# Kernel tuning notes

Hardware: AMD Instinct MI355X
Metric: run time of the kernel (lower is better)

The kernel has to match this reference:

```python
import jax, jax.numpy as jnp
import numpy as np

B, Q, D = 8, 1, 4096
NH, NKV, HD = 32, 8, 128
KV = 4096
ROPE_BASE = 10000.0


def setup_inputs() -> dict:
    key = jax.random.key(0)
    ks = jax.random.split(key, 10)
    s = 0.02  # realistic init scale for weights
    return {
        "hidden_states": jax.random.normal(ks[0], (B, Q, D), jnp.float32),
        "past_k": jax.random.normal(ks[1], (B, NH, KV, HD), jnp.float32),
        "past_v": jax.random.normal(ks[2], (B, NH, KV, HD), jnp.float32),
        "Wq": jax.random.normal(ks[3], (NH * HD, D), jnp.float32) * s,
        "bq": jax.random.normal(ks[4], (NH * HD,), jnp.float32) * s,
        "Wk": jax.random.normal(ks[5], (NKV * HD, D), jnp.float32) * s,
        "bk": jax.random.normal(ks[6], (NKV * HD,), jnp.float32) * s,
        "Wv": jax.random.normal(ks[7], (NKV * HD, D), jnp.float32) * s,
        "bv": jax.random.normal(ks[8], (NKV * HD,), jnp.float32) * s,
        "Wo": jax.random.normal(ks[9], (D, NH * HD), jnp.float32) * s,
        "position_ids": KV,  # current decode position (past length)
    }


def _rope(x, pos0):
    # x: [B, H, Q, HD]; rotate_half-style RoPE at positions pos0..pos0+Q-1
    half = HD // 2
    inv_freq = 1.0 / (ROPE_BASE ** (jnp.arange(half, dtype=jnp.float32) / half))
    pos = (pos0 + jnp.arange(Q)).astype(jnp.float32)          # [Q]
    ang = pos[:, None] * inv_freq[None, :]                    # [Q, half]
    cos = jnp.concatenate([jnp.cos(ang), jnp.cos(ang)], -1)   # [Q, HD]
    sin = jnp.concatenate([jnp.sin(ang), jnp.sin(ang)], -1)
    x1, x2 = x[..., :half], x[..., half:]
    rot = jnp.concatenate([-x2, x1], axis=-1)
    return x * cos + rot * sin


def reference(hidden_states, past_k, past_v, Wq, bq, Wk, bk, Wv, bv, Wo, position_ids):
    # QKV projections (Qwen: biased q/k/v, unbiased o)
    q = hidden_states @ Wq.T + bq   # [B, Q, NH*HD]
    k = hidden_states @ Wk.T + bk   # [B, Q, NKV*HD]
    v = hidden_states @ Wv.T + bv
    q = q.reshape(B, Q, NH, HD).transpose(0, 2, 1, 3)    # [B, NH, Q, HD]
    k = k.reshape(B, Q, NKV, HD).transpose(0, 2, 1, 3)   # [B, NKV, Q, HD]
    v = v.reshape(B, Q, NKV, HD).transpose(0, 2, 1, 3)
    # RoPE on current tokens only (past cache already rotated)
    q = _rope(q, position_ids)
    k = _rope(k, position_ids)
    # GQA repeat_interleave to full head count
    rep = NH // NKV
    k = jnp.repeat(k, rep, axis=1)   # [B, NH, Q, HD]
    v = jnp.repeat(v, rep, axis=1)
    # Assemble streaming KV window: past cache is stored post-repeat
    k = jnp.concatenate([past_k, k], axis=2)   # [B, NH, KV+Q, HD]
    v = jnp.concatenate([past_v, v], axis=2)
    scale = jnp.float32(1.0 / np.sqrt(HD))
    scores = jnp.einsum("bhqd,bhkd->bhqk", q, k) * scale   # [B, NH, Q, KV+Q]
    # causal: query positions KV..KV+Q-1 attend to key positions <= own pos
    qpos = KV + jnp.arange(Q)
    kpos = jnp.arange(KV + Q)
    mask = qpos[:, None] >= kpos[None, :]
    scores = jnp.where(mask, scores, jnp.float32(-1e30))
    attn = jax.nn.softmax(scores, axis=-1)
    ctx = jnp.einsum("bhqk,bhkd->bhqd", attn, v)           # [B, NH, Q, HD]
    ctx = ctx.transpose(0, 2, 1, 3).reshape(B, Q, NH * HD)
    return ctx @ Wo.T   # [B, Q, D]
```

## Files before the change

kernel.cpp:

```cpp
#include <hip/hip_runtime.h>
#include <hip/hip_bf16.h>
#include <math.h>

#define BB 8
#define DD 4096
#define NH 32
#define NKV 8
#define HD 128
#define KVL 4096
#define NSPLIT 16
#define CHUNK (KVL / NSPLIT)
#define SCALE 0.08838834764831845f

#define OFF_QRAW  0
#define OFF_KRAW  (OFF_QRAW + BB*NH*HD)
#define OFF_VRAW  (OFF_KRAW + BB*NKV*HD)
#define OFF_QROPE (OFF_VRAW + BB*NKV*HD)
#define OFF_KROPE (OFF_QROPE + BB*NH*HD)
#define OFF_PART  (OFF_KROPE + BB*NKV*HD)
#define PART_STRIDE 132
#define OFF_CTX   (OFF_PART + BB*NH*NSPLIT*PART_STRIDE)

__global__ __launch_bounds__(256) void k_qkv(
    const float* __restrict__ hs,
    const float* __restrict__ Wq, const float* __restrict__ bq,
    const float* __restrict__ Wk, const float* __restrict__ bk,
    const float* __restrict__ Wv, const float* __restrict__ bv,
    float* __restrict__ ws)
{
    const int wid  = threadIdx.x >> 6;
    const int lane = threadIdx.x & 63;
    const int row  = blockIdx.x * 4 + wid;
    const float* W; const float* bias; float* dst; int dstride; int r;
    if (row < 4096)      { W = Wq; bias = bq; r = row;        dst = ws + OFF_QRAW; dstride = NH*HD; }
    else if (row < 5120) { W = Wk; bias = bk; r = row - 4096; dst = ws + OFF_KRAW; dstride = NKV*HD; }
    else                 { W = Wv; bias = bv; r = row - 5120; dst = ws + OFF_VRAW; dstride = NKV*HD; }

    const float4* Wr = (const float4*)(W + (size_t)r * DD);
    float acc[BB];
    #pragma unroll
    for (int b = 0; b < BB; ++b) acc[b] = 0.f;

    for (int it = 0; it < DD/256; ++it) {
        const int idx = it*64 + lane;
        const float4 w4 = Wr[idx];
        #pragma unroll
        for (int b = 0; b < BB; ++b) {
            const float4 h4 = ((const float4*)(hs + (size_t)b*DD))[idx];
            acc[b] = fmaf(w4.x, h4.x, fmaf(w4.y, h4.y, fmaf(w4.z, h4.z, fmaf(w4.w, h4.w, acc[b]))));
        }
    }
    #pragma unroll
    for (int b = 0; b < BB; ++b) {
        float v = acc[b];
        #pragma unroll
        for (int off = 32; off; off >>= 1) v += __shfl_xor(v, off, 64);
        acc[b] = v;
    }
    if (lane == 0) {
        const float bb = bias[r];
        #pragma unroll
        for (int b = 0; b < BB; ++b) dst[(size_t)b*dstride + r] = acc[b] + bb;
    }
}

__global__ __launch_bounds__(256) void k_rope(const int* __restrict__ posp, float* __restrict__ ws)
{
    const int gid = blockIdx.x * 256 + threadIdx.x;
    const int i  = gid & (HD-1);
    const int hh = gid >> 7;
    const double pos = (double)posp[0];
    const int j = i & 63;
    const double ang = pos * pow(10000.0, -(double)j / 64.0);
    const float c = (float)cos(ang), s = (float)sin(ang);
    const bool isq = hh < BB*NH;
    const int hl = isq ? hh : hh - BB*NH;
    const float* src = ws + (isq ? OFF_QRAW  : OFF_KRAW)  + hl * HD;
    float* dstp      = ws + (isq ? OFF_QROPE : OFF_KROPE) + hl * HD;
    const float x = src[i];
    const float o = (i < 64) ? -src[i + 64] : src[i - 64];
    dstp[i] = fmaf(x, c, o * s);
}

__global__ __launch_bounds__(256) void k_attn(
    const float* __restrict__ Kc, const float* __restrict__ Vc,
    float* __restrict__ ws)
{
    __shared__ float sc[CHUNK + 1];
    __shared__ float red[4];
    __shared__ float ctxs[HD];

    const int pair  = blockIdx.x / NSPLIT;
    const int split = blockIdx.x % NSPLIT;
    const int b = pair >> 5, h = pair & 31;
    const int tid = threadIdx.x, wid = tid >> 6, lane = tid & 63;
    const int sub = lane >> 5, l32 = lane & 31;

    const float* q = ws + OFF_QROPE + pair * HD;
    const size_t base = ((size_t)pair * KVL + (size_t)split * CHUNK) * HD;
    const float* Kp = Kc + base;
    const float* Vp = Vc + base;
    const bool extra = (split == NSPLIT - 1);

    const float4 q4 = ((const float4*)q)[l32];

    #pragma unroll 4
    for (int it = 0; it < 32; ++it) {
        const int p = wid*64 + it*2 + sub;
        const float4 k4 = ((const float4*)(Kp + (size_t)p * HD))[l32];
        float v = q4.x*k4.x + q4.y*k4.y + q4.z*k4.z + q4.w*k4.w;
        #pragma unroll
        for (int off = 16; off; off >>= 1) v += __shfl_xor(v, off, 64);
        if (l32 == 0) sc[p] = v * SCALE;
    }
    if (extra && wid == 0) {
        const float* kn = ws + OFF_KROPE + (b*NKV + (h>>2)) * HD;
        const float4 k4 = ((const float4*)kn)[l32];
        float v = q4.x*k4.x + q4.y*k4.y + q4.z*k4.z + q4.w*k4.w;
        #pragma unroll
        for (int off = 16; off; off >>= 1) v += __shfl_xor(v, off, 64);
        if (lane == 0) sc[CHUNK] = v * SCALE;
    }
    __syncthreads();

    const int cnt = CHUNK + (extra ? 1 : 0);
    float m = -1e30f;
    for (int p2 = tid; p2 < cnt; p2 += 256) m = fmaxf(m, sc[p2]);
    #pragma unroll
    for (int off = 32; off; off >>= 1) m = fmaxf(m, __shfl_xor(m, off, 64));
    if (lane == 0) red[wid] = m;
    __syncthreads();
    m = fmaxf(fmaxf(red[0], red[1]), fmaxf(red[2], red[3]));
    __syncthreads();
    float lsum = 0.f;
    for (int p2 = tid; p2 < cnt; p2 += 256) {
        const float e = expf(sc[p2] - m);
        sc[p2] = e;
        lsum += e;
    }
    #pragma unroll
    for (int off = 32; off; off >>= 1) lsum += __shfl_xor(lsum, off, 64);
    if (lane == 0) red[wid] = lsum;
    __syncthreads();
    const float L = red[0] + red[1] + red[2] + red[3];

    const int d = tid & (HD-1);
    const int half = tid >> 7;
    float acc = 0.f;
    const float* Vh = Vp + (size_t)half * (CHUNK/2) * HD;
    for (int i2 = 0; i2 < CHUNK/2; ++i2)
        acc = fmaf(sc[half*(CHUNK/2) + i2], Vh[(size_t)i2 * HD + d], acc);
    if (extra && half == 0) {
        const float* vn = ws + OFF_VRAW + (b*NKV + (h>>2)) * HD;
        acc = fmaf(sc[CHUNK], vn[d], acc);
    }
    if (half == 0) ctxs[d] = acc;
    __syncthreads();
    if (half == 1) ctxs[d] += acc;
    __syncthreads();

    float* pp = ws + OFF_PART + ((size_t)pair * NSPLIT + split) * PART_STRIDE;
    if (tid < HD)            pp[tid]    = ctxs[tid];
    else if (tid == HD)      pp[HD]     = m;
    else if (tid == HD + 1)  pp[HD + 1] = L;
}

__global__ __launch_bounds__(128) void k_combine(float* __restrict__ ws)
{
    const int pair = blockIdx.x;
    const int d = threadIdx.x;
    const float* pp = ws + OFF_PART + (size_t)pair * NSPLIT * PART_STRIDE;
    __shared__ float sm[NSPLIT], sl[NSPLIT];
    if (d < NSPLIT) { sm[d] = pp[d*PART_STRIDE + HD]; sl[d] = pp[d*PART_STRIDE + HD + 1]; }
    __syncthreads();
    float M = -1e30f;
    #pragma unroll
    for (int s = 0; s < NSPLIT; ++s) M = fmaxf(M, sm[s]);
    float L = 0.f, acc = 0.f;
    #pragma unroll
    for (int s = 0; s < NSPLIT; ++s) {
        const float w = expf(sm[s] - M);
        L += sl[s] * w;
        acc += pp[s*PART_STRIDE + d] * w;
    }
    ws[OFF_CTX + pair*HD + d] = acc / L;
}

__global__ __launch_bounds__(256) void k_oproj(
    const float* __restrict__ Wo, const float* __restrict__ ws, float* __restrict__ out)
{
    const int wid  = threadIdx.x >> 6;
    const int lane = threadIdx.x & 63;
    const int row  = blockIdx.x * 4 + wid;
    const float4* Wr = (const float4*)(Wo + (size_t)row * DD);
    const float* ctx = ws + OFF_CTX;
    float acc[BB];
    #pragma unroll
    for (int b = 0; b < BB; ++b) acc[b] = 0.f;
    for (int it = 0; it < DD/256; ++it) {
        const int idx = it*64 + lane;
        const float4 w4 = Wr[idx];
        #pragma unroll
        for (int b = 0; b < BB; ++b) {
            const float4 h4 = ((const float4*)(ctx + (size_t)b*DD))[idx];
            acc[b] = fmaf(w4.x, h4.x, fmaf(w4.y, h4.y, fmaf(w4.z, h4.z, fmaf(w4.w, h4.w, acc[b]))));
        }
    }
    #pragma unroll
    for (int b = 0; b < BB; ++b) {
        float v = acc[b];
        #pragma unroll
        for (int off = 32; off; off >>= 1) v += __shfl_xor(v, off, 64);
        if (lane == 0) out[(size_t)b*DD + row] = v;
    }
}

extern "C" void kernel_launch(void* const* d_in, const int* in_sizes, int n_in,
                              void* d_out, int out_size, void* d_ws, size_t ws_size,
                              hipStream_t stream)
{
    const float* hs  = (const float*)d_in[0];
    const float* pk  = (const float*)d_in[1];
    const float* pv  = (const float*)d_in[2];
    const float* Wq  = (const float*)d_in[3];
    const float* bq  = (const float*)d_in[4];
    const float* Wk  = (const float*)d_in[5];
    const float* bk  = (const float*)d_in[6];
    const float* Wv  = (const float*)d_in[7];
    const float* bv  = (const float*)d_in[8];
    const float* Wo  = (const float*)d_in[9];
    const int*   pos = (const int*)d_in[10];
    float* out = (float*)d_out;
    float* ws  = (float*)d_ws;

    k_qkv   <<<6144/4,           256, 0, stream>>>(hs, Wq, bq, Wk, bk, Wv, bv, ws);
    k_rope  <<<(BB*(NH+NKV)*HD)/256, 256, 0, stream>>>(pos, ws);
    k_attn  <<<BB*NH*NSPLIT,     256, 0, stream>>>(pk, pv, ws);
    k_combine<<<BB*NH,           128, 0, stream>>>(ws);
    k_oproj <<<4096/4,           256, 0, stream>>>(Wo, ws, out);
}
```

Before: 271.0 us.

## Fuse RoPE into QKV projection and use per-wave online-softmax attention

The QKV projection kernel now has each wave compute the paired rows i and i+64 of a head and apply RoPE in registers, so the separate RoPE kernel and its workspace round trip go away. Attention is rewritten so each wavefront handles one split of 128 keys with a single-pass online softmax, reading K and V together. This removes the shared-memory score buffer and the block-level barriers. NSPLIT doubles to 32, which adds more partials for the combine kernel to merge, and the online softmax adds rescaling branches inside the inner loop.

```diff
diff --git a/kernel.cpp b/kernel.cpp
--- a/kernel.cpp
+++ b/kernel.cpp
@@ -4,165 +4,170 @@
 
 #define BB 8
 #define DD 4096
-#define NH 32
+#define NHQ 32
 #define NKV 8
 #define HD 128
 #define KVL 4096
-#define NSPLIT 16
+#define NSPLIT 32
 #define CHUNK (KVL / NSPLIT)
 #define SCALE 0.08838834764831845f
 
-#define OFF_QRAW  0
-#define OFF_KRAW  (OFF_QRAW + BB*NH*HD)
-#define OFF_VRAW  (OFF_KRAW + BB*NKV*HD)
-#define OFF_QROPE (OFF_VRAW + BB*NKV*HD)
-#define OFF_KROPE (OFF_QROPE + BB*NH*HD)
-#define OFF_PART  (OFF_KROPE + BB*NKV*HD)
+#define OFF_QROPE 0
+#define OFF_KROPE (OFF_QROPE + BB*NHQ*HD)
+#define OFF_VRAW  (OFF_KROPE + BB*NKV*HD)
+#define OFF_PART  (OFF_VRAW  + BB*NKV*HD)
 #define PART_STRIDE 132
-#define OFF_CTX   (OFF_PART + BB*NH*NSPLIT*PART_STRIDE)
+#define OFF_CTX   (OFF_PART + BB*NHQ*NSPLIT*PART_STRIDE)
 
 __global__ __launch_bounds__(256) void k_qkv(
     const float* __restrict__ hs,
     const float* __restrict__ Wq, const float* __restrict__ bq,
     const float* __restrict__ Wk, const float* __restrict__ bk,
     const float* __restrict__ Wv, const float* __restrict__ bv,
+    const int* __restrict__ posp,
     float* __restrict__ ws)
 {
     const int wid  = threadIdx.x >> 6;
     const int lane = threadIdx.x & 63;
-    const int row  = blockIdx.x * 4 + wid;
-    const float* W; const float* bias; float* dst; int dstride; int r;
-    if (row < 4096)      { W = Wq; bias = bq; r = row;        dst = ws + OFF_QRAW; dstride = NH*HD; }
-    else if (row < 5120) { W = Wk; bias = bk; r = row - 4096; dst = ws + OFF_KRAW; dstride = NKV*HD; }
-    else                 { W = Wv; bias = bv; r = row - 5120; dst = ws + OFF_VRAW; dstride = NKV*HD; }
-
-    const float4* Wr = (const float4*)(W + (size_t)r * DD);
-    float acc[BB];
-    #pragma unroll
-    for (int b = 0; b < BB; ++b) acc[b] = 0.f;
+    const int w    = blockIdx.x * 4 + wid;
+
+    const float* W; const float* bias; float* dst; int dstride; int r1; int i; bool rope;
+    if (w < 2048) {
+        const int h = w >> 6; i = w & 63; r1 = h*HD + i;
+        W = Wq; bias = bq; dst = ws + OFF_QROPE; dstride = NHQ*HD; rope = true;
+    } else if (w < 2560) {
+        const int w2 = w - 2048; const int h = w2 >> 6; i = w2 & 63; r1 = h*HD + i;
+        W = Wk; bias = bk; dst = ws + OFF_KROPE; dstride = NKV*HD; rope = true;
+    } else {
+        const int w3 = w - 2560; const int h = w3 >> 6; i = w3 & 63; r1 = h*HD + i;
+        W = Wv; bias = bv; dst = ws + OFF_VRAW; dstride = NKV*HD; rope = false;
+    }
+    const int r2 = r1 + 64;
+
+    const double pos = (double)posp[0];
+    const double ang = pos * pow(10000.0, -(double)i / 64.0);
+    const float c = (float)cos(ang), s = (float)sin(ang);
+
+    const float4* WrA = (const float4*)(W + (size_t)r1 * DD);
+    const float4* WrB = (const float4*)(W + (size_t)r2 * DD);
+    const float4* H   = (const float4*)hs;
+
+    float accA[BB], accB[BB];
+    #pragma unroll
+    for (int b = 0; b < BB; ++b) { accA[b] = 0.f; accB[b] = 0.f; }
 
     for (int it = 0; it < DD/256; ++it) {
         const int idx = it*64 + lane;
-        const float4 w4 = Wr[idx];
+        const float4 wa = WrA[idx];
+        const float4 wb = WrB[idx];
         #pragma unroll
         for (int b = 0; b < BB; ++b) {
-            const float4 h4 = ((const float4*)(hs + (size_t)b*DD))[idx];
-            acc[b] = fmaf(w4.x, h4.x, fmaf(w4.y, h4.y, fmaf(w4.z, h4.z, fmaf(w4.w, h4.w, acc[b]))));
+            const float4 h4 = H[b*(DD/4) + idx];
+            accA[b] = fmaf(wa.x, h4.x, fmaf(wa.y, h4.y, fmaf(wa.z, h4.z, fmaf(wa.w, h4.w, accA[b]))));
+            accB[b] = fmaf(wb.x, h4.x, fmaf(wb.y, h4.y, fmaf(wb.z, h4.z, fmaf(wb.w, h4.w, accB[b]))));
         }
     }
     #pragma unroll
     for (int b = 0; b < BB; ++b) {
-        float v = acc[b];
-        #pragma unroll
-        for (int off = 32; off; off >>= 1) v += __shfl_xor(v, off, 64);
-        acc[b] = v;
+        float va = accA[b], vb = accB[b];
+        #pragma unroll
+        for (int off = 32; off; off >>= 1) {
+            va += __shfl_xor(va, off, 64);
+            vb += __shfl_xor(vb, off, 64);
+        }
+        accA[b] = va; accB[b] = vb;
     }
     if (lane == 0) {
-        const float bb = bias[r];
-        #pragma unroll
-        for (int b = 0; b < BB; ++b) dst[(size_t)b*dstride + r] = acc[b] + bb;
-    }
-}
-
-__global__ __launch_bounds__(256) void k_rope(const int* __restrict__ posp, float* __restrict__ ws)
-{
-    const int gid = blockIdx.x * 256 + threadIdx.x;
-    const int i  = gid & (HD-1);
-    const int hh = gid >> 7;
-    const double pos = (double)posp[0];
-    const int j = i & 63;
-    const double ang = pos * pow(10000.0, -(double)j / 64.0);
-    const float c = (float)cos(ang), s = (float)sin(ang);
-    const bool isq = hh < BB*NH;
-    const int hl = isq ? hh : hh - BB*NH;
-    const float* src = ws + (isq ? OFF_QRAW  : OFF_KRAW)  + hl * HD;
-    float* dstp      = ws + (isq ? OFF_QROPE : OFF_KROPE) + hl * HD;
-    const float x = src[i];
-    const float o = (i < 64) ? -src[i + 64] : src[i - 64];
-    dstp[i] = fmaf(x, c, o * s);
+        const float b1 = bias[r1], b2 = bias[r2];
+        #pragma unroll
+        for (int b = 0; b < BB; ++b) {
+            const float a1 = accA[b] + b1;
+            const float a2 = accB[b] + b2;
+            float o1, o2;
+            if (rope) { o1 = fmaf(a1, c, -a2*s); o2 = fmaf(a2, c, a1*s); }
+            else      { o1 = a1;                 o2 = a2; }
+            dst[(size_t)b*dstride + r1] = o1;
+            dst[(size_t)b*dstride + r2] = o2;
+        }
+    }
 }
 
 __global__ __launch_bounds__(256) void k_attn(
     const float* __restrict__ Kc, const float* __restrict__ Vc,
     float* __restrict__ ws)
 {
-    __shared__ float sc[CHUNK + 1];
-    __shared__ float red[4];
-    __shared__ float ctxs[HD];
-
-    const int pair  = blockIdx.x / NSPLIT;
-    const int split = blockIdx.x % NSPLIT;
+    const int wid  = threadIdx.x >> 6;
+    const int lane = threadIdx.x & 63;
+    const int sub  = lane >> 5, l32 = lane & 31;
+    const int task  = blockIdx.x * 4 + wid;
+    const int pair  = task >> 5;
+    const int split = task & (NSPLIT - 1);
     const int b = pair >> 5, h = pair & 31;
-    const int tid = threadIdx.x, wid = tid >> 6, lane = tid & 63;
-    const int sub = lane >> 5, l32 = lane & 31;
-
-    const float* q = ws + OFF_QROPE + pair * HD;
+
+    const float4 q4 = ((const float4*)(ws + OFF_QROPE + (size_t)pair * HD))[l32];
     const size_t base = ((size_t)pair * KVL + (size_t)split * CHUNK) * HD;
-    const float* Kp = Kc + base;
-    const float* Vp = Vc + base;
-    const bool extra = (split == NSPLIT - 1);
-
-    const float4 q4 = ((const float4*)q)[l32];
+    const float4* Kp = (const float4*)(Kc + base);
+    const float4* Vp = (const float4*)(Vc + base);
+
+    float m = -1e30f, l = 0.f;
+    float4 acc = {0.f, 0.f, 0.f, 0.f};
 
     #pragma unroll 4
-    for (int it = 0; it < 32; ++it) {
-        const int p = wid*64 + it*2 + sub;
-        const float4 k4 = ((const float4*)(Kp + (size_t)p * HD))[l32];
-        float v = q4.x*k4.x + q4.y*k4.y + q4.z*k4.z + q4.w*k4.w;
-        #pragma unroll
-        for (int off = 16; off; off >>= 1) v += __shfl_xor(v, off, 64);
-        if (l32 == 0) sc[p] = v * SCALE;
-    }
-    if (extra && wid == 0) {
-        const float* kn = ws + OFF_KROPE + (b*NKV + (h>>2)) * HD;
-        const float4 k4 = ((const float4*)kn)[l32];
-        float v = q4.x*k4.x + q4.y*k4.y + q4.z*k4.z + q4.w*k4.w;
-        #pragma unroll
-        for (int off = 16; off; off >>= 1) v += __shfl_xor(v, off, 64);
-        if (lane == 0) sc[CHUNK] = v * SCALE;
-    }
-    __syncthreads();
-
-    const int cnt = CHUNK + (extra ? 1 : 0);
-    float m = -1e30f;
-    for (int p2 = tid; p2 < cnt; p2 += 256) m = fmaxf(m, sc[p2]);
-    #pragma unroll
-    for (int off = 32; off; off >>= 1) m = fmaxf(m, __shfl_xor(m, off, 64));
-    if (lane == 0) red[wid] = m;
-    __syncthreads();
-    m = fmaxf(fmaxf(red[0], red[1]), fmaxf(red[2], red[3]));
-    __syncthreads();
-    float lsum = 0.f;
-    for (int p2 = tid; p2 < cnt; p2 += 256) {
-        const float e = expf(sc[p2] - m);
-        sc[p2] = e;
-        lsum += e;
-    }
-    #pragma unroll
-    for (int off = 32; off; off >>= 1) lsum += __shfl_xor(lsum, off, 64);
-    if (lane == 0) red[wid] = lsum;
-    __syncthreads();
-    const float L = red[0] + red[1] + red[2] + red[3];
-
-    const int d = tid & (HD-1);
-    const int half = tid >> 7;
-    float acc = 0.f;
-    const float* Vh = Vp + (size_t)half * (CHUNK/2) * HD;
-    for (int i2 = 0; i2 < CHUNK/2; ++i2)
-        acc = fmaf(sc[half*(CHUNK/2) + i2], Vh[(size_t)i2 * HD + d], acc);
-    if (extra && half == 0) {
-        const float* vn = ws + OFF_VRAW + (b*NKV + (h>>2)) * HD;
-        acc = fmaf(sc[CHUNK], vn[d], acc);
-    }
-    if (half == 0) ctxs[d] = acc;
-    __syncthreads();
-    if (half == 1) ctxs[d] += acc;
-    __syncthreads();
-
-    float* pp = ws + OFF_PART + ((size_t)pair * NSPLIT + split) * PART_STRIDE;
-    if (tid < HD)            pp[tid]    = ctxs[tid];
-    else if (tid == HD)      pp[HD]     = m;
-    else if (tid == HD + 1)  pp[HD + 1] = L;
+    for (int it = 0; it < CHUNK/2; ++it) {
+        const int p = it*2 + sub;
+        const float4 k4 = Kp[p*32 + l32];
+        const float4 v4 = Vp[p*32 + l32];
+        float sv = fmaf(q4.x, k4.x, fmaf(q4.y, k4.y, fmaf(q4.z, k4.z, q4.w*k4.w)));
+        #pragma unroll
+        for (int off = 16; off; off >>= 1) sv += __shfl_xor(sv, off, 64);
+        sv *= SCALE;
+        if (sv > m) {
+            const float r_ = __expf(m - sv);
+            l *= r_; acc.x *= r_; acc.y *= r_; acc.z *= r_; acc.w *= r_;
+            m = sv;
+        }
+        const float pw = __expf(sv - m);
+        l += pw;
+        acc.x = fmaf(pw, v4.x, acc.x);
+        acc.y = fmaf(pw, v4.y, acc.y);
+        acc.z = fmaf(pw, v4.z, acc.z);
+        acc.w = fmaf(pw, v4.w, acc.w);
+    }
+
+    if (split == NSPLIT - 1 && sub == 0) {
+        const float4 k4 = ((const float4*)(ws + OFF_KROPE + (size_t)(b*NKV + (h>>2)) * HD))[l32];
+        const float4 v4 = ((const float4*)(ws + OFF_VRAW  + (size_t)(b*NKV + (h>>2)) * HD))[l32];
+        float sv = fmaf(q4.x, k4.x, fmaf(q4.y, k4.y, fmaf(q4.z, k4.z, q4.w*k4.w)));
+        #pragma unroll
+        for (int off = 16; off; off >>= 1) sv += __shfl_xor(sv, off, 64);
+        sv *= SCALE;
+        if (sv > m) {
+            const float r_ = __expf(m - sv);
+            l *= r_; acc.x *= r_; acc.y *= r_; acc.z *= r_; acc.w *= r_;
+            m = sv;
+        }
+        const float pw = __expf(sv - m);
+        l += pw;
+        acc.x = fmaf(pw, v4.x, acc.x);
+        acc.y = fmaf(pw, v4.y, acc.y);
+        acc.z = fmaf(pw, v4.z, acc.z);
+        acc.w = fmaf(pw, v4.w, acc.w);
+    }
+
+    const float M  = fmaxf(m, __shfl_xor(m, 32, 64));
+    const float r_ = __expf(m - M);
+    l *= r_; acc.x *= r_; acc.y *= r_; acc.z *= r_; acc.w *= r_;
+    l     += __shfl_xor(l,     32, 64);
+    acc.x += __shfl_xor(acc.x, 32, 64);
+    acc.y += __shfl_xor(acc.y, 32, 64);
+    acc.z += __shfl_xor(acc.z, 32, 64);
+    acc.w += __shfl_xor(acc.w, 32, 64);
+
+    if (sub == 0) {
+        float* pp = ws + OFF_PART + ((size_t)pair * NSPLIT + split) * PART_STRIDE;
+        ((float4*)pp)[l32] = acc;
+        if (l32 == 0) { pp[HD] = M; pp[HD+1] = l; }
+    }
 }
 
 __global__ __launch_bounds__(128) void k_combine(float* __restrict__ ws)
@@ -181,9 +186,9 @@
     for (int s = 0; s < NSPLIT; ++s) {
         const float w = expf(sm[s] - M);
         L += sl[s] * w;
-        acc += pp[s*PART_STRIDE + d] * w;
-    }
-    ws[OFF_CTX + pair*HD + d] = acc / L;
+        acc = fmaf(pp[s*PART_STRIDE + d], w, acc);
+    }
+    ws[OFF_CTX + (size_t)pair*HD + d] = acc / L;
 }
 
 __global__ __launch_bounds__(256) void k_oproj(
@@ -193,7 +198,7 @@
     const int lane = threadIdx.x & 63;
     const int row  = blockIdx.x * 4 + wid;
     const float4* Wr = (const float4*)(Wo + (size_t)row * DD);
-    const float* ctx = ws + OFF_CTX;
+    const float4* C  = (const float4*)(ws + OFF_CTX);
     float acc[BB];
     #pragma unroll
     for (int b = 0; b < BB; ++b) acc[b] = 0.f;
@@ -202,7 +207,7 @@
         const float4 w4 = Wr[idx];
         #pragma unroll
         for (int b = 0; b < BB; ++b) {
-            const float4 h4 = ((const float4*)(ctx + (size_t)b*DD))[idx];
+            const float4 h4 = C[b*(DD/4) + idx];
             acc[b] = fmaf(w4.x, h4.x, fmaf(w4.y, h4.y, fmaf(w4.z, h4.z, fmaf(w4.w, h4.w, acc[b]))));
         }
     }
@@ -233,9 +238,8 @@
     float* out = (float*)d_out;
     float* ws  = (float*)d_ws;
 
-    k_qkv   <<<6144/4,           256, 0, stream>>>(hs, Wq, bq, Wk, bk, Wv, bv, ws);
-    k_rope  <<<(BB*(NH+NKV)*HD)/256, 256, 0, stream>>>(pos, ws);
-    k_attn  <<<BB*NH*NSPLIT,     256, 0, stream>>>(pk, pv, ws);
-    k_combine<<<BB*NH,           128, 0, stream>>>(ws);
-    k_oproj <<<4096/4,           256, 0, stream>>>(Wo, ws, out);
-}
+    k_qkv    <<<3072/4,      256, 0, stream>>>(hs, Wq, bq, Wk, bk, Wv, bv, pos, ws);
+    k_attn   <<<BB*NHQ*NSPLIT/4, 256, 0, stream>>>(pk, pv, ws);
+    k_combine<<<BB*NHQ,      128, 0, stream>>>(ws);
+    k_oproj  <<<4096/4,      256, 0, stream>>>(Wo, ws, out);
+}
```

Measured after the change: 268.7 us. Within noise of the previous version (-0.9%).
